# Performance work log

Measured on AMD Instinct MI355X. Metric: run time of the kernel, lower is better.

## Reference

```python
import jax, jax.numpy as jnp
import numpy as np

EPS = 1e-8

def setup_inputs() -> dict:
    key = jax.random.key(0)
    k1, k2, k3 = jax.random.split(key, 3)
    B, N, M = 4, 8192, 8192
    source = jax.random.normal(k1, (B, N, 3), dtype=jnp.float32)
    target = jax.random.normal(k2, (B, M, 3), dtype=jnp.float32)
    weights = jax.random.uniform(k3, (B, N), dtype=jnp.float32)
    return {"source": source, "target": target, "weights": weights}

def reference(source, target, weights):
    # Pairwise squared distances: (B, N, M)
    diff = source[:, :, None, :] - target[:, None, :, :]
    sq_distances = jnp.sum(diff * diff, axis=-1)
    # squared=False -> take sqrt with eps for stability
    distances = jnp.sqrt(sq_distances + EPS)
    # source -> target nearest-neighbor distance, weighted
    s2t = jnp.min(distances, axis=2) * weights  # (B, N)
    forward_loss = jnp.mean(s2t)
    # symmetric=True: target -> source (unweighted, as in original)
    t2s = jnp.min(distances, axis=1)  # (B, M)
    backward_loss = jnp.mean(t2s)
    return forward_loss + backward_loss
```

## Files before the change

### kernel.cpp

```cpp
#include <hip/hip_runtime.h>
#include <math.h>


#define EPS 1e-8f

typedef _Float16 f16x8 __attribute__((ext_vector_type(8)));
typedef float    f32x16 __attribute__((ext_vector_type(16)));

constexpr int B_    = 4;
constexpr int N_    = 8192;
constexpr int TPB   = 256;
constexpr int QPW   = 64;
constexpr int QPB   = 4 * QPW;
constexpr int RCH   = 8;
constexpr int CHUNK = N_ / RCH;
constexpr int RB    = 64;

#define FOLD(d, ma, mb)                                         \
    _Pragma("unroll")                                           \
    for (int r = 0; r < 8; r += 2)                              \
        ma = fminf(fminf(d[r], d[r + 1]), ma);                  \
    _Pragma("unroll")                                           \
    for (int r = 8; r < 16; r += 2)                             \
        mb = fminf(fminf(d[r], d[r + 1]), mb);

__global__ __launch_bounds__(TPB, 4)
void nn_mfma_kernel(const float* __restrict__ src, const float* __restrict__ tgt,
                    float* __restrict__ part, float* __restrict__ out)
{
    __shared__ f16x8 sref[CHUNK + 64];

    if (blockIdx.x == 0 && blockIdx.y == 0 && blockIdx.z == 0 && threadIdx.x == 0)
        out[0] = 0.f;

    const int zb  = blockIdx.z;
    const int dir = zb >> 2;
    const int b   = zb & 3;
    const float* Rraw = (dir ? src : tgt) + ((size_t)b * N_ + (size_t)blockIdx.y * CHUNK) * 3;
    const float* Qraw = (dir ? tgt : src) + (size_t)b * N_ * 3;
    float* opart = part + ((size_t)zb * RCH + blockIdx.y) * N_;

    const int tid = threadIdx.x;
    const _Float16 h0 = (_Float16)0.f;
    const _Float16 h1 = (_Float16)1.f;

    for (int k = tid; k < CHUNK; k += TPB) {
        const float* rp = Rraw + (size_t)k * 3;
        _Float16 hx = (_Float16)rp[0], hy = (_Float16)rp[1], hz = (_Float16)rp[2];
        float fx = (float)hx, fy = (float)hy, fz = (float)hz;
        float rsq = fx * fx + fy * fy + fz * fz;
        _Float16 rh = (_Float16)rsq;
        _Float16 rl = (_Float16)(rsq - (float)rh);
        f16x8 a = {(_Float16)(-2.f * fx), (_Float16)(-2.f * fy),
                   (_Float16)(-2.f * fz), rh, rl, h0, h0, h0};
        sref[k] = a;
    }
    if (tid < 64) {
        f16x8 z = {h0, h0, h0, h0, h0, h0, h0, h0};
        sref[CHUNK + tid] = z;
    }

    const int lane = tid & 63;
    const int wv   = tid >> 6;
    const int l31  = lane & 31;
    const int half = lane >> 5;
    const int qb   = blockIdx.x * QPB + wv * QPW;

    f16x8 B0 = {h0, h0, h0, h0, h0, h0, h0, h0};
    f16x8 B1 = B0;
    float qs0 = 0.f, qs1 = 0.f;
    if (half == 0) {
        const float* q0 = Qraw + (size_t)(qb + l31) * 3;
        const float* q1 = Qraw + (size_t)(qb + 32 + l31) * 3;
        _Float16 ax = (_Float16)q0[0], ay = (_Float16)q0[1], az = (_Float16)q0[2];
        _Float16 bx = (_Float16)q1[0], by = (_Float16)q1[1], bz = (_Float16)q1[2];
        float fax = (float)ax, fay = (float)ay, faz = (float)az;
        float fbx = (float)bx, fby = (float)by, fbz = (float)bz;
        B0 = f16x8{ax, ay, az, h1, h1, h0, h0, h0};
        B1 = f16x8{bx, by, bz, h1, h1, h0, h0, h0};
        qs0 = fax * fax + fay * fay + faz * faz;
        qs1 = fbx * fbx + fby * fby + fbz * fbz;
    }
    __syncthreads();

    const f32x16 zc = {};

    int idx = (half == 0) ? l31 : CHUNK;
    const int step = (half == 0) ? 32 : 0;
    float mn0a = 3.0e38f, mn0b = 3.0e38f, mn1a = 3.0e38f, mn1b = 3.0e38f;

    f16x8 a = sref[idx];
    idx += step;
    f32x16 dA0 = __builtin_amdgcn_mfma_f32_32x32x16_f16(a, B0, zc, 0, 0, 0);
    f32x16 dA1 = __builtin_amdgcn_mfma_f32_32x32x16_f16(a, B1, zc, 0, 0, 0);
    a = sref[idx];
    idx += step;
    for (int s = 0; s < 15; ++s) {
        f32x16 dB0 = __builtin_amdgcn_mfma_f32_32x32x16_f16(a, B0, zc, 0, 0, 0);
        f32x16 dB1 = __builtin_amdgcn_mfma_f32_32x32x16_f16(a, B1, zc, 0, 0, 0);
        a = sref[idx];
        idx += step;
        FOLD(dA0, mn0a, mn0b)
        FOLD(dA1, mn1a, mn1b)
        dA0 = __builtin_amdgcn_mfma_f32_32x32x16_f16(a, B0, zc, 0, 0, 0);
        dA1 = __builtin_amdgcn_mfma_f32_32x32x16_f16(a, B1, zc, 0, 0, 0);
        a = sref[idx];
        idx += step;
        FOLD(dB0, mn0a, mn0b)
        FOLD(dB1, mn1a, mn1b)
    }
    {
        f32x16 dB0 = __builtin_amdgcn_mfma_f32_32x32x16_f16(a, B0, zc, 0, 0, 0);
        f32x16 dB1 = __builtin_amdgcn_mfma_f32_32x32x16_f16(a, B1, zc, 0, 0, 0);
        FOLD(dA0, mn0a, mn0b)
        FOLD(dA1, mn1a, mn1b)
        FOLD(dB0, mn0a, mn0b)
        FOLD(dB1, mn1a, mn1b)
    }

    float mn0 = fminf(mn0a, mn0b);
    float mn1 = fminf(mn1a, mn1b);
    mn0 = fminf(mn0, __shfl_xor(mn0, 32));
    mn1 = fminf(mn1, __shfl_xor(mn1, 32));
    if (half == 0) {
        opart[qb + l31]      = fmaxf(mn0 + qs0, 0.f);
        opart[qb + 32 + l31] = fmaxf(mn1 + qs1, 0.f);
    }
}

__global__ __launch_bounds__(TPB)
void reduce_kernel(const float* __restrict__ part,
                   const float* __restrict__ w,
                   float* __restrict__ out)
{
    const int Q = 2 * B_ * N_;
    const float invBN = 1.0f / (float)(B_ * N_);

    float sum = 0.0f;
    for (int t = blockIdx.x * TPB + threadIdx.x; t < Q; t += RB * TPB) {
        const int zb = t >> 13;
        const int qn = t & (N_ - 1);
        const float* p = part + ((size_t)zb * RCH) * N_ + qn;
        float m = p[0];
#pragma unroll
        for (int c = 1; c < RCH; ++c) m = fminf(m, p[(size_t)c * N_]);
        float d = sqrtf(m + EPS);
        sum += (zb < 4) ? d * w[(size_t)zb * N_ + qn] : d;
    }
    sum *= invBN;

    __shared__ float ss[TPB / 64];
    int lane = threadIdx.x & 63;
    int wid  = threadIdx.x >> 6;
#pragma unroll
    for (int off = 32; off > 0; off >>= 1) sum += __shfl_down(sum, off);
    if (lane == 0) ss[wid] = sum;
    __syncthreads();
    if (threadIdx.x == 0) {
        float s = 0.0f;
#pragma unroll
        for (int i = 0; i < TPB / 64; ++i) s += ss[i];
        atomicAdd(out, s);
    }
}

extern "C" void kernel_launch(void* const* d_in, const int* in_sizes, int n_in,
                              void* d_out, int out_size, void* d_ws, size_t ws_size,
                              hipStream_t stream)
{
    const float* src = (const float*)d_in[0];
    const float* tgt = (const float*)d_in[1];
    const float* w   = (const float*)d_in[2];
    float* out = (float*)d_out;

    float* part = (float*)d_ws;

    dim3 grid(N_ / QPB, RCH, 2 * B_);
    nn_mfma_kernel<<<grid, TPB, 0, stream>>>(src, tgt, part, out);

    reduce_kernel<<<RB, TPB, 0, stream>>>(part, w, out);
}
```

Baseline: 75.20 us.

## Fuse final reduction into NN kernel via last-block atomic counters

Removes the separate reduce kernel launch. Each query-tile group counts finished reference chunks with an atomic counter, and the last block to finish does the min over chunks, the sqrt, the weighting and a block sum, then adds the result atomically into a global accumulator. A second global counter lets the final block write the output. In exchange it adds a hipMemsetAsync on every call, thread fences and atomics. The tail work is now spread across the main kernel's blocks instead of running as a separate launch.

```diff
diff --git a/kernel.cpp b/kernel.cpp
--- a/kernel.cpp
+++ b/kernel.cpp
@@ -14,7 +14,7 @@
 constexpr int QPB   = 4 * QPW;
 constexpr int RCH   = 8;
 constexpr int CHUNK = N_ / RCH;
-constexpr int RB    = 64;
+constexpr int NGRP  = 8 * 32;
 
 #define FOLD(d, ma, mb)                                         \
     _Pragma("unroll")                                           \
@@ -26,12 +26,13 @@
 
 __global__ __launch_bounds__(TPB, 4)
 void nn_mfma_kernel(const float* __restrict__ src, const float* __restrict__ tgt,
-                    float* __restrict__ part, float* __restrict__ out)
+                    const float* __restrict__ w, float* __restrict__ part,
+                    unsigned* __restrict__ counters, float* __restrict__ fsum,
+                    float* __restrict__ out)
 {
     __shared__ f16x8 sref[CHUNK + 64];
-
-    if (blockIdx.x == 0 && blockIdx.y == 0 && blockIdx.z == 0 && threadIdx.x == 0)
-        out[0] = 0.f;
+    __shared__ float ss[TPB / 64];
+    __shared__ int   isLast;
 
     const int zb  = blockIdx.z;
     const int dir = zb >> 2;
@@ -126,41 +127,37 @@
         opart[qb + l31]      = fmaxf(mn0 + qs0, 0.f);
         opart[qb + 32 + l31] = fmaxf(mn1 + qs1, 0.f);
     }
-}
 
-__global__ __launch_bounds__(TPB)
-void reduce_kernel(const float* __restrict__ part,
-                   const float* __restrict__ w,
-                   float* __restrict__ out)
-{
-    const int Q = 2 * B_ * N_;
-    const float invBN = 1.0f / (float)(B_ * N_);
+    __threadfence();
+    __syncthreads();
+    if (tid == 0) {
+        unsigned old = atomicAdd(&counters[zb * 32 + blockIdx.x], 1u);
+        isLast = (old == RCH - 1);
+    }
+    __syncthreads();
+    if (!isLast) return;
 
-    float sum = 0.0f;
-    for (int t = blockIdx.x * TPB + threadIdx.x; t < Q; t += RB * TPB) {
-        const int zb = t >> 13;
-        const int qn = t & (N_ - 1);
-        const float* p = part + ((size_t)zb * RCH) * N_ + qn;
-        float m = p[0];
+    __threadfence();
+    const int qn = blockIdx.x * QPB + tid;
+    const float* p = part + ((size_t)zb * RCH) * N_ + qn;
+    float m = p[0];
 #pragma unroll
-        for (int c = 1; c < RCH; ++c) m = fminf(m, p[(size_t)c * N_]);
-        float d = sqrtf(m + EPS);
-        sum += (zb < 4) ? d * w[(size_t)zb * N_ + qn] : d;
-    }
-    sum *= invBN;
-
-    __shared__ float ss[TPB / 64];
-    int lane = threadIdx.x & 63;
-    int wid  = threadIdx.x >> 6;
+    for (int c = 1; c < RCH; ++c) m = fminf(m, p[(size_t)c * N_]);
+    float d = sqrtf(m + EPS);
+    float val = dir ? d : d * w[(size_t)b * N_ + qn];
 #pragma unroll
-    for (int off = 32; off > 0; off >>= 1) sum += __shfl_down(sum, off);
-    if (lane == 0) ss[wid] = sum;
+    for (int off = 32; off > 0; off >>= 1) val += __shfl_down(val, off);
+    if (lane == 0) ss[wv] = val;
     __syncthreads();
-    if (threadIdx.x == 0) {
-        float s = 0.0f;
-#pragma unroll
-        for (int i = 0; i < TPB / 64; ++i) s += ss[i];
-        atomicAdd(out, s);
+    if (tid == 0) {
+        float s = ss[0] + ss[1] + ss[2] + ss[3];
+        atomicAdd(fsum, s * (1.0f / (float)(B_ * N_)));
+        __threadfence();
+        unsigned og = atomicAdd(&counters[NGRP], 1u);
+        if (og == NGRP - 1) {
+            __threadfence();
+            out[0] = atomicAdd(fsum, 0.0f);
+        }
     }
 }
 
@@ -173,10 +170,12 @@
     const float* w   = (const float*)d_in[2];
     float* out = (float*)d_out;
 
-    float* part = (float*)d_ws;
+    float*    part     = (float*)d_ws;
+    unsigned* counters = (unsigned*)((char*)d_ws + (size_t)2 * B_ * RCH * N_ * 4);
+    float*    fsum     = (float*)(counters + NGRP + 1);
+
+    hipMemsetAsync(counters, 0, (NGRP + 2) * sizeof(unsigned), stream);
 
     dim3 grid(N_ / QPB, RCH, 2 * B_);
-    nn_mfma_kernel<<<grid, TPB, 0, stream>>>(src, tgt, part, out);
-
-    reduce_kernel<<<RB, TPB, 0, stream>>>(part, w, out);
+    nn_mfma_kernel<<<grid, TPB, 0, stream>>>(src, tgt, w, part, counters, fsum, out);
 }
```

After: 217.8 us. +189.6%, slower.
